# Kernel tuning notes

Measured on AMD Instinct MI355X. Metric: run time of the kernel, lower is better.

## Reference

```python
import jax, jax.numpy as jnp
import numpy as np

S, B, D = 2048, 2, 2048      # seq, batch, hidden  (x is [S, B, D])
H, KV, HD = 16, 4, 128        # n_head, n_kv_head, head_dim
N_REP = H // KV               # GQA repeat factor
THETA = 10000.0


def setup_inputs() -> dict:
    key = jax.random.key(0)
    ks = jax.random.split(key, 5)
    sc = 1.0 / np.sqrt(D)
    x = jax.random.normal(ks[0], (S, B, D), jnp.float32)
    Wq = jax.random.normal(ks[1], (D, H * HD), jnp.float32) * sc
    Wk = jax.random.normal(ks[2], (D, KV * HD), jnp.float32) * sc
    Wv = jax.random.normal(ks[3], (D, KV * HD), jnp.float32) * sc
    Wo = jax.random.normal(ks[4], (H * HD, D), jnp.float32) * sc
    return {"x": x, "Wq": Wq, "Wk": Wk, "Wv": Wv, "Wo": Wo}


def _rope_cos_sin(seq_len, dim, theta):
    inv_freq = 1.0 / (theta ** (jnp.arange(0, dim, 2, dtype=jnp.float32) / dim))
    t = jnp.arange(seq_len, dtype=jnp.float32)
    freqs = jnp.outer(t, inv_freq)                  # [S, dim/2]
    emb = jnp.concatenate([freqs, freqs], axis=-1)  # [S, dim]
    return jnp.cos(emb), jnp.sin(emb)


def _rotate_half(u):
    u1, u2 = jnp.split(u, 2, axis=-1)
    return jnp.concatenate([-u2, u1], axis=-1)


def reference(x, Wq, Wk, Wv, Wo):
    # projections (torch Linear without bias; W stored as [in, out] here)
    q = (x @ Wq).reshape(S, B, H, HD)
    k = (x @ Wk).reshape(S, B, KV, HD)
    v = (x @ Wv).reshape(S, B, KV, HD)

    # RoPE (full rotary, partial_rotary_factor == 1.0)
    cos, sin = _rope_cos_sin(S, HD, THETA)
    cos = cos[:, None, None, :]  # [S,1,1,HD] broadcasts over B, heads
    sin = sin[:, None, None, :]
    q = q * cos + _rotate_half(q) * sin
    k = k * cos + _rotate_half(k) * sin

    # GQA: repeat_interleave kv heads to match query heads
    k = jnp.repeat(k, N_REP, axis=2)
    v = jnp.repeat(v, N_REP, axis=2)

    # [S,B,H,HD] -> [B,H,S,HD]
    q = q.transpose(1, 2, 0, 3)
    k = k.transpose(1, 2, 0, 3)
    v = v.transpose(1, 2, 0, 3)

    # causal SDPA (dropout_p = 0 in eval)
    scale = 1.0 / np.sqrt(HD)
    scores = jnp.einsum('bhqd,bhkd->bhqk', q, k) * scale
    causal = jnp.tril(jnp.ones((S, S), dtype=bool))
    scores = jnp.where(causal, scores, jnp.finfo(scores.dtype).min)
    probs = jax.nn.softmax(scores, axis=-1)
    out = jnp.einsum('bhqk,bhkd->bhqd', probs, v)

    # [B,H,S,HD] -> [S,B,D], then output projection
    out = out.transpose(2, 0, 1, 3).reshape(S, B, D)
    return out @ Wo
```

## Files before the change

kernel.cpp:

```cpp
#include <hip/hip_runtime.h>
#include <hip/hip_bf16.h>
#include <cstdint>
#include <math.h>

#define S_LEN   2048
#define B_SZ    2
#define D_MODEL 2048
#define NH      16
#define NKV     4
#define HD      128
#define ROWS    (S_LEN * B_SZ)
#define NQKV    3072
#define SCALE   0.08838834764831845f

typedef __attribute__((ext_vector_type(8))) short short8;
typedef __attribute__((ext_vector_type(4))) float f32x4;

__device__ __forceinline__ short f2bf(float f) {
  union { float f; unsigned u; } v; v.f = f;
  unsigned r = v.u + 0x7fffu + ((v.u >> 16) & 1u);
  return (short)(r >> 16);
}
__device__ __forceinline__ float bf2f(short x) {
  union { unsigned u; float f; } v;
  v.u = ((unsigned)(unsigned short)x) << 16;
  return v.f;
}

__device__ __forceinline__ void async16(const short* g, short* l) {
  __builtin_amdgcn_global_load_lds(
      (const __attribute__((address_space(1))) void*)(uintptr_t)(const void*)g,
      (__attribute__((address_space(3))) void*)(uintptr_t)(void*)l,
      16, 0, 0);
}

__global__ void cvt_bf16_kernel(const float* __restrict__ src, short* __restrict__ dst, int n4) {
  int t = blockIdx.x * blockDim.x + threadIdx.x;
  if (t >= n4) return;
  float4 v = ((const float4*)src)[t];
  short4 o;
  o.x = f2bf(v.x); o.y = f2bf(v.y); o.z = f2bf(v.z); o.w = f2bf(v.w);
  *(short4*)(dst + (size_t)t * 4) = o;
}

__global__ void wtrans_kernel(const float* __restrict__ src, short* __restrict__ dst,
                              int Kdim, int Ndim) {
  __shared__ float tile[32][33];
  int n0 = blockIdx.x * 32, k0 = blockIdx.y * 32;
  for (int r = threadIdx.y; r < 32; r += 8)
    tile[r][threadIdx.x] = src[(size_t)(k0 + r) * Ndim + n0 + threadIdx.x];
  __syncthreads();
  for (int r = threadIdx.y; r < 32; r += 8)
    dst[(size_t)(n0 + r) * Kdim + k0 + threadIdx.x] = f2bf(tile[threadIdx.x][r]);
}

#define BM 128
#define BN 128
#define BK 32

template<int BF16OUT>
__global__ __launch_bounds__(256) void gemm_bt_kernel(const short* __restrict__ A,
    const short* __restrict__ Bt, void* __restrict__ Cv, int M, int N, int K) {
  __shared__ alignas(16) short As[BM * BK];
  __shared__ alignas(16) short Bs[BN * BK];
  const int tid  = threadIdx.x;
  const int wave = tid >> 6;
  const int lane = tid & 63;
  const int quad = lane >> 4;
  const int lr   = lane & 15;
  const int m0 = blockIdx.y * BM;
  const int n0 = blockIdx.x * BN;
  const int wm = (wave >> 1) * 64;
  const int wn = (wave & 1) * 64;

  f32x4 acc[4][4];
#pragma unroll
  for (int i = 0; i < 4; i++)
#pragma unroll
    for (int j = 0; j < 4; j++) acc[i][j] = (f32x4){0.f, 0.f, 0.f, 0.f};

  const int r0 = tid >> 2,          c0 = (tid & 3) * 8;
  const int r1 = (tid + 256) >> 2,  c1 = (tid & 3) * 8;

  for (int kt = 0; kt < K; kt += BK) {
    const short* ga = A  + (size_t)m0 * K + kt;
    const short* gb = Bt + (size_t)n0 * K + kt;
    async16(ga + (size_t)r0 * K + c0, As + wave * 512);
    async16(ga + (size_t)r1 * K + c1, As + 2048 + wave * 512);
    async16(gb + (size_t)r0 * K + c0, Bs + wave * 512);
    async16(gb + (size_t)r1 * K + c1, Bs + 2048 + wave * 512);
    __syncthreads();

    short8 a[4], b[4];
#pragma unroll
    for (int i = 0; i < 4; i++) a[i] = *(const short8*)(As + (wm + i * 16 + lr) * BK + quad * 8);
#pragma unroll
    for (int j = 0; j < 4; j++) b[j] = *(const short8*)(Bs + (wn + j * 16 + lr) * BK + quad * 8);
#pragma unroll
    for (int i = 0; i < 4; i++)
#pragma unroll
      for (int j = 0; j < 4; j++)
        acc[i][j] = __builtin_amdgcn_mfma_f32_16x16x32_bf16(a[i], b[j], acc[i][j], 0, 0, 0);
    __syncthreads();
  }

#pragma unroll
  for (int i = 0; i < 4; i++) {
    const int row = m0 + wm + i * 16 + quad * 4;
#pragma unroll
    for (int j = 0; j < 4; j++) {
      const int col = n0 + wn + j * 16 + lr;
#pragma unroll
      for (int r = 0; r < 4; r++) {
        float v = acc[i][j][r];
        if (BF16OUT) ((short*)Cv)[(size_t)(row + r) * N + col] = f2bf(v);
        else         ((float*)Cv)[(size_t)(row + r) * N + col] = v;
      }
    }
  }
}

__global__ void rope_kernel(const short* __restrict__ QKVb, short* __restrict__ Qb,
                            short* __restrict__ Kpack) {
  const int head = blockIdx.y;
  const int t = blockIdx.x * blockDim.x + threadIdx.x;
  const int i = t & 63;
  const int row = t >> 6;
  const int s = row >> 1;
  const int b = row & 1;
  float inv_freq = expf(-(float)i * (1.0f / 64.0f) * 9.210340371976184f);
  float ang = (float)s * inv_freq;
  float sn, cs;
  sincosf(ang, &sn, &cs);
  if (head < NH) {
    const short* p = QKVb + (size_t)row * NQKV + head * HD;
    float v1 = bf2f(p[i]), v2 = bf2f(p[i + 64]);
    short* q = Qb + ((size_t)(b * NH + head) * S_LEN + s) * HD;
    q[i]      = f2bf((v1 * cs - v2 * sn) * SCALE);
    q[i + 64] = f2bf((v2 * cs + v1 * sn) * SCALE);
  } else {
    const int kv = head - NH;
    const short* p = QKVb + (size_t)row * NQKV + NH * HD + kv * HD;
    float v1 = bf2f(p[i]), v2 = bf2f(p[i + 64]);
    float k1 = v1 * cs - v2 * sn;
    float k2 = v2 * cs + v1 * sn;
    short* kp = Kpack + (size_t)(b * NKV + kv) * S_LEN * HD;
    const int tile = s >> 4, lrr = s & 15;
    const int d1 = i, d2 = i + 64;
    kp[(size_t)((tile * 4 + (d1 >> 5)) * 64 + ((d1 >> 3) & 3) * 16 + lrr) * 8 + (d1 & 7)] = f2bf(k1);
    kp[(size_t)((tile * 4 + (d2 >> 5)) * 64 + ((d2 >> 3) & 3) * 16 + lrr) * 8 + (d2 & 7)] = f2bf(k2);
  }
}

__global__ void vtrans_kernel(const short* __restrict__ QKVb, short* __restrict__ Vtb) {
  __shared__ short tile[32][33];
  const int bz = blockIdx.z;
  const int b  = bz >> 2;
  const int s0 = blockIdx.x * 32;
  const int d0 = blockIdx.y * 32;
  const int vcol = NH * HD + NKV * HD + (bz & 3) * HD;
  for (int r = threadIdx.y; r < 32; r += 8)
    tile[r][threadIdx.x] = QKVb[(size_t)((s0 + r) * B_SZ + b) * NQKV + vcol + d0 + threadIdx.x];
  __syncthreads();
  for (int r = threadIdx.y; r < 32; r += 8)
    Vtb[((size_t)bz * HD + d0 + r) * S_LEN + s0 + threadIdx.x] = tile[threadIdx.x][r];
}

__global__ void vpack_kernel(const short* __restrict__ Vtb, short* __restrict__ Vpack) {
  const int tid = threadIdx.x, wave = tid >> 6, lane = tid & 63;
  const int quad = lane >> 4, lr = lane & 15;
  const int chunk = blockIdx.x & 63, stream = blockIdx.x >> 6;
  const short* src = Vtb + (size_t)stream * HD * S_LEN;
  short* dst = Vpack + (size_t)stream * HD * S_LEN + chunk * 4096 + lane * 8;
#pragma unroll
  for (int k = 0; k < 2; ++k) {
    const int dt = wave + k * 4;
    short8 v = *(const short8*)(src + (size_t)(dt * 16 + lr) * S_LEN + chunk * 32 + quad * 8);
    *(short8*)(dst + dt * 512) = v;
  }
}

#define PSP 72

template<bool MASK>
__device__ __forceinline__ void attn_iter64(
    const short* __restrict__ Kpk, const short* __restrict__ Vpk,
    short* __restrict__ Psw, const short8 qf[4], int kv0, int nt, int qlim,
    int quad, int lr, f32x4 o[8], float& m_i, float& l_i)
{
  const int lane_off = (quad * 16 + lr) * 8;
  short8 kf[4][4];
#pragma unroll
  for (int t = 0; t < 4; ++t)
    if (t < nt) {
      const short* kp = Kpk + (size_t)((kv0 >> 4) + t) * 2048 + lane_off;
#pragma unroll
      for (int c = 0; c < 4; ++c)
        kf[t][c] = *(const short8*)(kp + c * 512);
    }
  f32x4 sc[4];
#pragma unroll
  for (int t = 0; t < 4; ++t) {
    if (t < nt) {
      f32x4 s = (f32x4){0.f, 0.f, 0.f, 0.f};
#pragma unroll
      for (int c = 0; c < 4; ++c)
        s = __builtin_amdgcn_mfma_f32_16x16x32_bf16(kf[t][c], qf[c], s, 0, 0, 0);
      sc[t] = s;
    } else {
      sc[t] = (f32x4){-3.0e38f, -3.0e38f, -3.0e38f, -3.0e38f};
    }
  }
  const bool c1v = !MASK || (nt > 2);
  short8 vf0[8], vf1[8];
  const short* vp = Vpk + (size_t)(kv0 >> 5) * 4096 + lane_off;
#pragma unroll
  for (int dt = 0; dt < 8; ++dt) vf0[dt] = *(const short8*)(vp + dt * 512);
  if (c1v) {
#pragma unroll
    for (int dt = 0; dt < 8; ++dt) vf1[dt] = *(const short8*)(vp + 4096 + dt * 512);
  }
  if (MASK) {
#pragma unroll
    for (int t = 0; t < 4; ++t)
#pragma unroll
      for (int r = 0; r < 4; ++r)
        if (kv0 + t * 16 + quad * 4 + r > qlim) sc[t][r] = -3.0e38f;
  }
  float mb = -3.0e38f;
#pragma unroll
  for (int t = 0; t < 4; ++t)
#pragma unroll
    for (int r = 0; r < 4; ++r) mb = fmaxf(mb, sc[t][r]);
  mb = fmaxf(mb, __shfl_xor(mb, 16, 64));
  mb = fmaxf(mb, __shfl_xor(mb, 32, 64));
  const float mnew = fmaxf(m_i, mb);
  const float alpha = __expf(m_i - mnew);
  m_i = mnew;
  float rs = 0.f;
#pragma unroll
  for (int t = 0; t < 4; ++t) {
    short4 pw;
    float p0 = __expf(sc[t][0] - mnew);
    float p1 = __expf(sc[t][1] - mnew);
    float p2 = __expf(sc[t][2] - mnew);
    float p3 = __expf(sc[t][3] - mnew);
    rs += (p0 + p1) + (p2 + p3);
    pw.x = f2bf(p0); pw.y = f2bf(p1); pw.z = f2bf(p2); pw.w = f2bf(p3);
    *(short4*)(Psw + lr * PSP + t * 16 + quad * 4) = pw;
  }
  rs += __shfl_xor(rs, 16, 64);
  rs += __shfl_xor(rs, 32, 64);
  l_i = l_i * alpha + rs;
#pragma unroll
  for (int n = 0; n < 8; ++n)
#pragma unroll
    for (int r = 0; r < 4; ++r) o[n][r] *= alpha;
  short8 pb0 = *(const short8*)(Psw + lr * PSP + quad * 8);
#pragma unroll
  for (int dt = 0; dt < 8; ++dt)
    o[dt] = __builtin_amdgcn_mfma_f32_16x16x32_bf16(vf0[dt], pb0, o[dt], 0, 0, 0);
  if (c1v) {
    short8 pb1 = *(const short8*)(Psw + lr * PSP + 32 + quad * 8);
#pragma unroll
    for (int dt = 0; dt < 8; ++dt)
      o[dt] = __builtin_amdgcn_mfma_f32_16x16x32_bf16(vf1[dt], pb1, o[dt], 0, 0, 0);
  }
}

__global__ __launch_bounds__(256) void attn_kernel(const short* __restrict__ Qb,
    const short* __restrict__ Kpack, const short* __restrict__ Vpack,
    short* __restrict__ Ob) {
  __shared__ alignas(16) short Ps[4][16 * PSP];
  const int tid = threadIdx.x, wave = tid >> 6, lane = tid & 63;
  const int quad = lane >> 4, lr = lane & 15;
  const int bid = blockIdx.x;
  const int sid  = bid & 7;
  const int hsub = (bid >> 3) & 3;
  const int qg   = 31 - (bid >> 5);
  const int b = sid >> 2, kvh = sid & 3;
  const int h = kvh * 4 + hsub;
  const int qw = (qg * 4 + wave) * 16;

  const short* Qp  = Qb    + ((size_t)(b * NH + h) * S_LEN + qw) * HD;
  const short* Kpk = Kpack + (size_t)(b * NKV + kvh) * S_LEN * HD;
  const short* Vpk = Vpack + (size_t)(b * NKV + kvh) * HD * S_LEN;
  short* Psw = &Ps[wave][0];

  short8 qf[4];
#pragma unroll
  for (int c = 0; c < 4; ++c)
    qf[c] = *(const short8*)(Qp + lr * HD + c * 32 + quad * 8);

  f32x4 o[8];
#pragma unroll
  for (int n = 0; n < 8; ++n) o[n] = (f32x4){0.f, 0.f, 0.f, 0.f};
  float m_i = -3.0e38f, l_i = 0.f;

  const int full = qw >> 6;
  const int qlim = qw + lr;
  for (int it = 0; it < full; ++it)
    attn_iter64<false>(Kpk, Vpk, Psw, qf, it * 64, 4, qlim, quad, lr, o, m_i, l_i);
  attn_iter64<true>(Kpk, Vpk, Psw, qf, full * 64, ((qw & 63) >> 4) + 1, qlim,
                    quad, lr, o, m_i, l_i);

  const float invl = 1.0f / l_i;
  short* op = Ob + ((size_t)(qw + lr) * B_SZ + b) * D_MODEL + h * HD + quad * 4;
#pragma unroll
  for (int dt = 0; dt < 8; ++dt) {
    short4 ov;
    ov.x = f2bf(o[dt][0] * invl);
    ov.y = f2bf(o[dt][1] * invl);
    ov.z = f2bf(o[dt][2] * invl);
    ov.w = f2bf(o[dt][3] * invl);
    *(short4*)(op + dt * 16) = ov;
  }
}

extern "C" void kernel_launch(void* const* d_in, const int* in_sizes, int n_in,
                              void* d_out, int out_size, void* d_ws, size_t ws_size,
                              hipStream_t stream) {
  (void)in_sizes; (void)n_in; (void)out_size; (void)ws_size;
  const float* x  = (const float*)d_in[0];
  const float* Wq = (const float*)d_in[1];
  const float* Wk = (const float*)d_in[2];
  const float* Wv = (const float*)d_in[3];
  const float* Wo = (const float*)d_in[4];
  float* out = (float*)d_out;
  char* ws = (char*)d_ws;

  short* Wqkv_t = (short*)(ws);
  short* xb     = (short*)(ws + 12582912);
  short* Qb     = (short*)(ws);
  short* Kpack  = (short*)(ws + 16777216);
  short* Vtb    = (short*)(ws + 20971520);
  short* Vpack  = (short*)(ws + 25165824);
  short* QKVb   = (short*)(ws + 29360128);
  short* Ob     = (short*)(ws + 29360128);
  short* Wo_t   = (short*)(ws + 54525952);

  dim3 tblk(32, 8);

  cvt_bf16_kernel<<<(ROWS * D_MODEL / 4 + 255) / 256, 256, 0, stream>>>(x, xb, ROWS * D_MODEL / 4);
  wtrans_kernel<<<dim3(64, 64), tblk, 0, stream>>>(Wq, Wqkv_t,               2048, 2048);
  wtrans_kernel<<<dim3(16, 64), tblk, 0, stream>>>(Wk, Wqkv_t + 2048 * 2048, 2048,  512);
  wtrans_kernel<<<dim3(16, 64), tblk, 0, stream>>>(Wv, Wqkv_t + 2560 * 2048, 2048,  512);
  wtrans_kernel<<<dim3(64, 64), tblk, 0, stream>>>(Wo, Wo_t,                 2048, 2048);
  gemm_bt_kernel<1><<<dim3(NQKV / BN, ROWS / BM), 256, 0, stream>>>(xb, Wqkv_t, QKVb, ROWS, NQKV, D_MODEL);
  rope_kernel<<<dim3(1024, NH + NKV), 256, 0, stream>>>(QKVb, Qb, Kpack);
  vtrans_kernel<<<dim3(S_LEN / 32, HD / 32, B_SZ * NKV), tblk, 0, stream>>>(QKVb, Vtb);
  vpack_kernel<<<dim3(512), 256, 0, stream>>>(Vtb, Vpack);
  attn_kernel<<<dim3(1024), 256, 0, stream>>>(Qb, Kpack, Vpack, Ob);
  gemm_bt_kernel<0><<<dim3(D_MODEL / BN, ROWS / BM), 256, 0, stream>>>(Ob, Wo_t, out, ROWS, D_MODEL, D_MODEL);
}
```

Measured before the change: 350.2 us.

## Process two GQA query heads per wave and fuse V transpose with packing

Each attention wave now handles two query heads sharing the same KV head, so every K and V fragment load feeds two MFMAs. This halves the number of attention blocks and the K/V global traffic per head. The register footprint doubles (two output accumulators), which the launch bound of 2 constrains and which may cause spills or lower occupancy. Separately, the V transpose kernel and the pack kernel are merged into one kernel that transposes through shared memory, removing an intermediate buffer round trip and a launch.

```diff
diff --git a/kernel.cpp b/kernel.cpp
--- a/kernel.cpp
+++ b/kernel.cpp
@@ -152,81 +152,35 @@
   }
 }
 
-__global__ void vtrans_kernel(const short* __restrict__ QKVb, short* __restrict__ Vtb) {
-  __shared__ short tile[32][33];
-  const int bz = blockIdx.z;
-  const int b  = bz >> 2;
-  const int s0 = blockIdx.x * 32;
-  const int d0 = blockIdx.y * 32;
-  const int vcol = NH * HD + NKV * HD + (bz & 3) * HD;
-  for (int r = threadIdx.y; r < 32; r += 8)
-    tile[r][threadIdx.x] = QKVb[(size_t)((s0 + r) * B_SZ + b) * NQKV + vcol + d0 + threadIdx.x];
+__global__ void vpack_kernel(const short* __restrict__ QKVb, short* __restrict__ Vpack) {
+  __shared__ short tile[32][136];
+  const int tid = threadIdx.x;
+  const int chunk = blockIdx.x & 63, stream = blockIdx.x >> 6;
+  const int b = stream >> 2, kv = stream & 3;
+  const int vcol = NH * HD + NKV * HD + kv * HD;
+  {
+    const int r = tid >> 3, c = (tid & 7) * 16;
+    const short* src = QKVb + (size_t)((chunk * 32 + r) * B_SZ + b) * NQKV + vcol + c;
+    *(short8*)(&tile[r][c])     = *(const short8*)(src);
+    *(short8*)(&tile[r][c + 8]) = *(const short8*)(src + 8);
+  }
   __syncthreads();
-  for (int r = threadIdx.y; r < 32; r += 8)
-    Vtb[((size_t)bz * HD + d0 + r) * S_LEN + s0 + threadIdx.x] = tile[threadIdx.x][r];
-}
-
-__global__ void vpack_kernel(const short* __restrict__ Vtb, short* __restrict__ Vpack) {
-  const int tid = threadIdx.x, wave = tid >> 6, lane = tid & 63;
-  const int quad = lane >> 4, lr = lane & 15;
-  const int chunk = blockIdx.x & 63, stream = blockIdx.x >> 6;
-  const short* src = Vtb + (size_t)stream * HD * S_LEN;
+  const int wave = tid >> 6, lane = tid & 63, quad = lane >> 4, lr = lane & 15;
   short* dst = Vpack + (size_t)stream * HD * S_LEN + chunk * 4096 + lane * 8;
 #pragma unroll
   for (int k = 0; k < 2; ++k) {
     const int dt = wave + k * 4;
-    short8 v = *(const short8*)(src + (size_t)(dt * 16 + lr) * S_LEN + chunk * 32 + quad * 8);
+    short8 v;
+#pragma unroll
+    for (int j = 0; j < 8; ++j) v[j] = tile[quad * 8 + j][dt * 16 + lr];
     *(short8*)(dst + dt * 512) = v;
   }
 }
 
 #define PSP 72
 
-template<bool MASK>
-__device__ __forceinline__ void attn_iter64(
-    const short* __restrict__ Kpk, const short* __restrict__ Vpk,
-    short* __restrict__ Psw, const short8 qf[4], int kv0, int nt, int qlim,
-    int quad, int lr, f32x4 o[8], float& m_i, float& l_i)
-{
-  const int lane_off = (quad * 16 + lr) * 8;
-  short8 kf[4][4];
-#pragma unroll
-  for (int t = 0; t < 4; ++t)
-    if (t < nt) {
-      const short* kp = Kpk + (size_t)((kv0 >> 4) + t) * 2048 + lane_off;
-#pragma unroll
-      for (int c = 0; c < 4; ++c)
-        kf[t][c] = *(const short8*)(kp + c * 512);
-    }
-  f32x4 sc[4];
-#pragma unroll
-  for (int t = 0; t < 4; ++t) {
-    if (t < nt) {
-      f32x4 s = (f32x4){0.f, 0.f, 0.f, 0.f};
-#pragma unroll
-      for (int c = 0; c < 4; ++c)
-        s = __builtin_amdgcn_mfma_f32_16x16x32_bf16(kf[t][c], qf[c], s, 0, 0, 0);
-      sc[t] = s;
-    } else {
-      sc[t] = (f32x4){-3.0e38f, -3.0e38f, -3.0e38f, -3.0e38f};
-    }
-  }
-  const bool c1v = !MASK || (nt > 2);
-  short8 vf0[8], vf1[8];
-  const short* vp = Vpk + (size_t)(kv0 >> 5) * 4096 + lane_off;
-#pragma unroll
-  for (int dt = 0; dt < 8; ++dt) vf0[dt] = *(const short8*)(vp + dt * 512);
-  if (c1v) {
-#pragma unroll
-    for (int dt = 0; dt < 8; ++dt) vf1[dt] = *(const short8*)(vp + 4096 + dt * 512);
-  }
-  if (MASK) {
-#pragma unroll
-    for (int t = 0; t < 4; ++t)
-#pragma unroll
-      for (int r = 0; r < 4; ++r)
-        if (kv0 + t * 16 + quad * 4 + r > qlim) sc[t][r] = -3.0e38f;
-  }
+__device__ __forceinline__ float softmax_store(const f32x4 sc[4], float& m_i,
+    float& l_i, short* __restrict__ Psw, int quad, int lr) {
   float mb = -3.0e38f;
 #pragma unroll
   for (int t = 0; t < 4; ++t)
@@ -252,68 +206,130 @@
   rs += __shfl_xor(rs, 16, 64);
   rs += __shfl_xor(rs, 32, 64);
   l_i = l_i * alpha + rs;
+  return alpha;
+}
+
+template<bool MASK>
+__device__ __forceinline__ void attn_iter64_2h(
+    const short* __restrict__ Kpk, const short* __restrict__ Vpk,
+    short* __restrict__ Psw0, short* __restrict__ Psw1,
+    const short8 qf0[4], const short8 qf1[4], int kv0, int nt, int qlim,
+    int quad, int lr, f32x4 o0[8], f32x4 o1[8],
+    float& m_0, float& l_0, float& m_1, float& l_1)
+{
+  const int lane_off = (quad * 16 + lr) * 8;
+  f32x4 s0[4], s1[4];
+#pragma unroll
+  for (int t = 0; t < 4; ++t) {
+    if (t < nt) {
+      const short* kp = Kpk + (size_t)((kv0 >> 4) + t) * 2048 + lane_off;
+      f32x4 a0 = (f32x4){0.f, 0.f, 0.f, 0.f};
+      f32x4 a1 = (f32x4){0.f, 0.f, 0.f, 0.f};
+#pragma unroll
+      for (int c = 0; c < 4; ++c) {
+        short8 kf = *(const short8*)(kp + c * 512);
+        a0 = __builtin_amdgcn_mfma_f32_16x16x32_bf16(kf, qf0[c], a0, 0, 0, 0);
+        a1 = __builtin_amdgcn_mfma_f32_16x16x32_bf16(kf, qf1[c], a1, 0, 0, 0);
+      }
+      s0[t] = a0; s1[t] = a1;
+    } else {
+      s0[t] = (f32x4){-3.0e38f, -3.0e38f, -3.0e38f, -3.0e38f};
+      s1[t] = s0[t];
+    }
+  }
+  if (MASK) {
+#pragma unroll
+    for (int t = 0; t < 4; ++t)
+#pragma unroll
+      for (int r = 0; r < 4; ++r)
+        if (kv0 + t * 16 + quad * 4 + r > qlim) { s0[t][r] = -3.0e38f; s1[t][r] = -3.0e38f; }
+  }
+  const float al0 = softmax_store(s0, m_0, l_0, Psw0, quad, lr);
+  const float al1 = softmax_store(s1, m_1, l_1, Psw1, quad, lr);
 #pragma unroll
   for (int n = 0; n < 8; ++n)
 #pragma unroll
-    for (int r = 0; r < 4; ++r) o[n][r] *= alpha;
-  short8 pb0 = *(const short8*)(Psw + lr * PSP + quad * 8);
-#pragma unroll
-  for (int dt = 0; dt < 8; ++dt)
-    o[dt] = __builtin_amdgcn_mfma_f32_16x16x32_bf16(vf0[dt], pb0, o[dt], 0, 0, 0);
-  if (c1v) {
-    short8 pb1 = *(const short8*)(Psw + lr * PSP + 32 + quad * 8);
-#pragma unroll
-    for (int dt = 0; dt < 8; ++dt)
-      o[dt] = __builtin_amdgcn_mfma_f32_16x16x32_bf16(vf1[dt], pb1, o[dt], 0, 0, 0);
-  }
-}
-
-__global__ __launch_bounds__(256) void attn_kernel(const short* __restrict__ Qb,
+    for (int r = 0; r < 4; ++r) { o0[n][r] *= al0; o1[n][r] *= al1; }
+  const short* vp = Vpk + (size_t)(kv0 >> 5) * 4096 + lane_off;
+  short8 pb0 = *(const short8*)(Psw0 + lr * PSP + quad * 8);
+  short8 pb1 = *(const short8*)(Psw1 + lr * PSP + quad * 8);
+#pragma unroll
+  for (int dt = 0; dt < 8; ++dt) {
+    short8 vf = *(const short8*)(vp + dt * 512);
+    o0[dt] = __builtin_amdgcn_mfma_f32_16x16x32_bf16(vf, pb0, o0[dt], 0, 0, 0);
+    o1[dt] = __builtin_amdgcn_mfma_f32_16x16x32_bf16(vf, pb1, o1[dt], 0, 0, 0);
+  }
+  if (!MASK || nt > 2) {
+    short8 pc0 = *(const short8*)(Psw0 + lr * PSP + 32 + quad * 8);
+    short8 pc1 = *(const short8*)(Psw1 + lr * PSP + 32 + quad * 8);
+#pragma unroll
+    for (int dt = 0; dt < 8; ++dt) {
+      short8 vf = *(const short8*)(vp + 4096 + dt * 512);
+      o0[dt] = __builtin_amdgcn_mfma_f32_16x16x32_bf16(vf, pc0, o0[dt], 0, 0, 0);
+      o1[dt] = __builtin_amdgcn_mfma_f32_16x16x32_bf16(vf, pc1, o1[dt], 0, 0, 0);
+    }
+  }
+}
+
+__global__ __launch_bounds__(256, 2) void attn_kernel(const short* __restrict__ Qb,
     const short* __restrict__ Kpack, const short* __restrict__ Vpack,
     short* __restrict__ Ob) {
-  __shared__ alignas(16) short Ps[4][16 * PSP];
+  __shared__ alignas(16) short Ps[4][2][16 * PSP];
   const int tid = threadIdx.x, wave = tid >> 6, lane = tid & 63;
   const int quad = lane >> 4, lr = lane & 15;
   const int bid = blockIdx.x;
-  const int sid  = bid & 7;
-  const int hsub = (bid >> 3) & 3;
-  const int qg   = 31 - (bid >> 5);
+  const int sid = bid & 7;
+  const int hp  = (bid >> 3) & 1;
+  const int qg  = 31 - (bid >> 4);
   const int b = sid >> 2, kvh = sid & 3;
-  const int h = kvh * 4 + hsub;
+  const int h0 = kvh * 4 + hp * 2;
   const int qw = (qg * 4 + wave) * 16;
 
-  const short* Qp  = Qb    + ((size_t)(b * NH + h) * S_LEN + qw) * HD;
+  const short* Qp0 = Qb    + ((size_t)(b * NH + h0) * S_LEN + qw) * HD;
+  const short* Qp1 = Qp0   + (size_t)S_LEN * HD;
   const short* Kpk = Kpack + (size_t)(b * NKV + kvh) * S_LEN * HD;
   const short* Vpk = Vpack + (size_t)(b * NKV + kvh) * HD * S_LEN;
-  short* Psw = &Ps[wave][0];
-
-  short8 qf[4];
-#pragma unroll
-  for (int c = 0; c < 4; ++c)
-    qf[c] = *(const short8*)(Qp + lr * HD + c * 32 + quad * 8);
-
-  f32x4 o[8];
-#pragma unroll
-  for (int n = 0; n < 8; ++n) o[n] = (f32x4){0.f, 0.f, 0.f, 0.f};
-  float m_i = -3.0e38f, l_i = 0.f;
+  short* Psw0 = &Ps[wave][0][0];
+  short* Psw1 = &Ps[wave][1][0];
+
+  short8 qf0[4], qf1[4];
+#pragma unroll
+  for (int c = 0; c < 4; ++c) {
+    qf0[c] = *(const short8*)(Qp0 + lr * HD + c * 32 + quad * 8);
+    qf1[c] = *(const short8*)(Qp1 + lr * HD + c * 32 + quad * 8);
+  }
+
+  f32x4 o0[8], o1[8];
+#pragma unroll
+  for (int n = 0; n < 8; ++n) { o0[n] = (f32x4){0.f, 0.f, 0.f, 0.f}; o1[n] = o0[n]; }
+  float m_0 = -3.0e38f, l_0 = 0.f, m_1 = -3.0e38f, l_1 = 0.f;
 
   const int full = qw >> 6;
   const int qlim = qw + lr;
   for (int it = 0; it < full; ++it)
-    attn_iter64<false>(Kpk, Vpk, Psw, qf, it * 64, 4, qlim, quad, lr, o, m_i, l_i);
-  attn_iter64<true>(Kpk, Vpk, Psw, qf, full * 64, ((qw & 63) >> 4) + 1, qlim,
-                    quad, lr, o, m_i, l_i);
-
-  const float invl = 1.0f / l_i;
-  short* op = Ob + ((size_t)(qw + lr) * B_SZ + b) * D_MODEL + h * HD + quad * 4;
+    attn_iter64_2h<false>(Kpk, Vpk, Psw0, Psw1, qf0, qf1, it * 64, 4, qlim,
+                          quad, lr, o0, o1, m_0, l_0, m_1, l_1);
+  attn_iter64_2h<true>(Kpk, Vpk, Psw0, Psw1, qf0, qf1, full * 64,
+                       ((qw & 63) >> 4) + 1, qlim, quad, lr, o0, o1,
+                       m_0, l_0, m_1, l_1);
+
+  const float invl0 = 1.0f / l_0;
+  const float invl1 = 1.0f / l_1;
+  short* op0 = Ob + ((size_t)(qw + lr) * B_SZ + b) * D_MODEL + h0 * HD + quad * 4;
 #pragma unroll
   for (int dt = 0; dt < 8; ++dt) {
     short4 ov;
-    ov.x = f2bf(o[dt][0] * invl);
-    ov.y = f2bf(o[dt][1] * invl);
-    ov.z = f2bf(o[dt][2] * invl);
-    ov.w = f2bf(o[dt][3] * invl);
-    *(short4*)(op + dt * 16) = ov;
+    ov.x = f2bf(o0[dt][0] * invl0);
+    ov.y = f2bf(o0[dt][1] * invl0);
+    ov.z = f2bf(o0[dt][2] * invl0);
+    ov.w = f2bf(o0[dt][3] * invl0);
+    *(short4*)(op0 + dt * 16) = ov;
+    short4 ow;
+    ow.x = f2bf(o1[dt][0] * invl1);
+    ow.y = f2bf(o1[dt][1] * invl1);
+    ow.z = f2bf(o1[dt][2] * invl1);
+    ow.w = f2bf(o1[dt][3] * invl1);
+    *(short4*)(op0 + HD + dt * 16) = ow;
   }
 }
 
@@ -333,7 +349,6 @@
   short* xb     = (short*)(ws + 12582912);
   short* Qb     = (short*)(ws);
   short* Kpack  = (short*)(ws + 16777216);
-  short* Vtb    = (short*)(ws + 20971520);
   short* Vpack  = (short*)(ws + 25165824);
   short* QKVb   = (short*)(ws + 29360128);
   short* Ob     = (short*)(ws + 29360128);
@@ -348,8 +363,7 @@
   wtrans_kernel<<<dim3(64, 64), tblk, 0, stream>>>(Wo, Wo_t,                 2048, 2048);
   gemm_bt_kernel<1><<<dim3(NQKV / BN, ROWS / BM), 256, 0, stream>>>(xb, Wqkv_t, QKVb, ROWS, NQKV, D_MODEL);
   rope_kernel<<<dim3(1024, NH + NKV), 256, 0, stream>>>(QKVb, Qb, Kpack);
-  vtrans_kernel<<<dim3(S_LEN / 32, HD / 32, B_SZ * NKV), tblk, 0, stream>>>(QKVb, Vtb);
-  vpack_kernel<<<dim3(512), 256, 0, stream>>>(Vtb, Vpack);
-  attn_kernel<<<dim3(1024), 256, 0, stream>>>(Qb, Kpack, Vpack, Ob);
+  vpack_kernel<<<dim3(512), 256, 0, stream>>>(QKVb, Vpack);
+  attn_kernel<<<dim3(512), 256, 0, stream>>>(Qb, Kpack, Vpack, Ob);
   gemm_bt_kernel<0><<<dim3(D_MODEL / BN, ROWS / BM), 256, 0, stream>>>(Ob, Wo_t, out, ROWS, D_MODEL, D_MODEL);
 }
```

New measurement: 433.4 us. 1.24x slower.
